# Performance work log

Measured on AMD Instinct MI355X. Metric: run time of the kernel, lower is better.

Reference implementation:

```python
import jax, jax.numpy as jnp
import numpy as np

T = 2048        # tokens
HID = 4096      # hidden_size
H = 32          # num attention heads
KV = 8          # num key/value heads (GQA)
D = HID // H    # head_dim = 128
THETA = 10000.0


def setup_inputs() -> dict:
    key = jax.random.key(0)
    k1, k2, k3 = jax.random.split(key, 3)
    hidden_states = jax.random.normal(k1, (T, HID), jnp.float32)
    positions = jnp.arange(T, dtype=jnp.int32)
    Wqkv = jax.random.normal(k2, ((H + 2 * KV) * D, HID), jnp.float32) * 0.02
    Wo = jax.random.normal(k3, (HID, H * D), jnp.float32) * 0.02
    return {"hidden_states": hidden_states, "positions": positions,
            "Wqkv": Wqkv, "Wo": Wo}


def _rope(positions, x):
    """Neox-style rotary embedding. x: [T, h, D], positions: [T]."""
    half = D // 2
    inv_freq = 1.0 / (THETA ** (jnp.arange(half, dtype=jnp.float32) / half))
    ang = positions.astype(jnp.float32)[:, None] * inv_freq      # [T, half]
    cos = jnp.cos(ang)[:, None, :]                                # [T, 1, half]
    sin = jnp.sin(ang)[:, None, :]
    x1, x2 = x[..., :half], x[..., half:]
    return jnp.concatenate([x1 * cos - x2 * sin, x2 * cos + x1 * sin], axis=-1)


def reference(hidden_states, positions, Wqkv, Wo):
    # fused QKV projection (no bias)
    qkv = hidden_states @ Wqkv.T                                  # [T, (H+2KV)*D]
    q, k, v = jnp.split(qkv, [H * D, H * D + KV * D], axis=1)
    q = q.reshape(T, H, D)
    k = k.reshape(T, KV, D)
    v = v.reshape(T, KV, D)
    # RoPE on q and k
    q = _rope(positions, q)
    k = _rope(positions, k)
    # GQA: expand kv heads to match q heads
    g = H // KV
    k = jnp.repeat(k, g, axis=1)                                  # [T, H, D]
    v = jnp.repeat(v, g, axis=1)
    # causal attention (flash-attention math)
    scores = jnp.einsum('thd,shd->hts', q, k) * (D ** -0.5)       # [H, T, T]
    causal = jnp.tril(jnp.ones((T, T), dtype=bool))
    scores = jnp.where(causal[None], scores, jnp.float32(-1e30))
    probs = jax.nn.softmax(scores, axis=-1)
    attn = jnp.einsum('hts,shd->thd', probs, v).reshape(T, H * D)
    # output projection
    return attn @ Wo.T
```

## Files before the change

kernel.cpp:

```cpp
#include <hip/hip_runtime.h>
#include <stdint.h>

#define T_SEQ 2048
#define HIDDEN 4096
#define NHEAD 32
#define NKV 8
#define HDIM 128
#define QKVN 6144

typedef __bf16 bf16x8 __attribute__((ext_vector_type(8)));
typedef float f32x4 __attribute__((ext_vector_type(4)));
typedef unsigned short u16;
typedef u16 u16x8 __attribute__((ext_vector_type(8)));
typedef u16 u16x4 __attribute__((ext_vector_type(4)));

__device__ __forceinline__ u16 f2bf(float f) {
  uint32_t u = __builtin_bit_cast(uint32_t, f);
  u = (u + 0x7fffu + ((u >> 16) & 1u)) >> 16;
  return (u16)u;
}
__device__ __forceinline__ float bf2f(u16 h) {
  uint32_t u = ((uint32_t)h) << 16;
  return __builtin_bit_cast(float, u);
}

__device__ __forceinline__ void gload16(const void* g, void* l) {
  __builtin_amdgcn_global_load_lds(
      (__attribute__((address_space(1))) void*)(uintptr_t)g,
      (__attribute__((address_space(3))) void*)(uintptr_t)l, 16, 0, 0);
}

__global__ void cvt_f32_bf16(const float* __restrict__ in, u16* __restrict__ out, int n) {
  int i = (blockIdx.x * blockDim.x + threadIdx.x) * 4;
  int stride = gridDim.x * blockDim.x * 4;
  for (; i < n; i += stride) {
    float4 v = *(const float4*)(in + i);
    u16x4 o;
    o.x = f2bf(v.x); o.y = f2bf(v.y); o.z = f2bf(v.z); o.w = f2bf(v.w);
    *(u16x4*)(out + i) = o;
  }
}

__global__ void rope_kernel(u16* __restrict__ qkv, const int* __restrict__ pos) {
  int idx = blockIdx.x * blockDim.x + threadIdx.x;
  if (idx >= T_SEQ * 40 * 64) return;
  int i = idx & 63;
  int head = (idx >> 6) % 40;
  int t = idx / (40 * 64);
  int base = head < NHEAD ? head * HDIM : NHEAD * HDIM + (head - NHEAD) * HDIM;
  float p = (float)pos[t];
  float inv_freq = exp2f(-(float)i * (13.287712379549449f / 64.0f));
  float ang = p * inv_freq;
  float s, c;
  sincosf(ang, &s, &c);
  u16* p1 = qkv + (size_t)t * QKVN + base + i;
  u16* p2 = p1 + 64;
  float x1 = bf2f(*p1), x2 = bf2f(*p2);
  *p1 = f2bf(x1 * c - x2 * s);
  *p2 = f2bf(x2 * c + x1 * s);
}

__device__ __forceinline__ void storeC(float* p, float v) { *p = v; }
__device__ __forceinline__ void storeC(u16* p, float v) { *p = f2bf(v); }

template <typename OutT>
__global__ void __launch_bounds__(256, 3)
gemm_k32(const u16* __restrict__ A, const u16* __restrict__ B,
         OutT* __restrict__ C, int M, int N, int K,
         int nbx, int rw, int rh) {
  __shared__ u16 As_[3][128 * 32];
  __shared__ u16 Bs_[3][128 * 32];

  const int tid = threadIdx.x;
  const int lane = tid & 63;
  const int w = tid >> 6;
  const int wr = w >> 1, wc = w & 1;
  const int l15 = lane & 15, lg = lane >> 4;

  const int c8 = blockIdx.x & 7;
  const int i8 = blockIdx.x >> 3;
  const int rpr = nbx / rw;
  const int by = (c8 / rpr) * rh + (i8 % rh);
  const int bx = (c8 % rpr) * rw + (i8 / rh);
  const int bm = by * 128, bn = bx * 128;

  const u16* asrc[2];
  const u16* bsrc[2];
#pragma unroll
  for (int g = 0; g < 2; ++g) {
    int u = g * 256 + w * 64 + lane;
    int r = u >> 2;
    int s = (u & 3) ^ (r & 3) ^ ((r >> 2) & 3);
    asrc[g] = A + (size_t)(bm + r) * K + s * 8;
    bsrc[g] = B + (size_t)(bn + r) * K + s * 8;
  }

  const int sl = (lg ^ (l15 & 3) ^ ((l15 >> 2) & 3)) * 8;
  const int a_rd = (wr * 64 + l15) * 32 + sl;
  const int b_rd = (wc * 64 + l15) * 32 + sl;

  f32x4 acc[4][4] = {};

#define BARRIER() asm volatile("s_barrier" ::: "memory")
#define WAITBAR(n_) asm volatile("s_waitcnt vmcnt(" #n_ ")\n\ts_barrier" ::: "memory")
#define STAGE(t_, p_)                                                          \
  {                                                                            \
    gload16(asrc[0] + (size_t)(t_) * 32, &As_[p_][w * 512]);                   \
    gload16(asrc[1] + (size_t)(t_) * 32, &As_[p_][2048 + w * 512]);            \
    gload16(bsrc[0] + (size_t)(t_) * 32, &Bs_[p_][w * 512]);                   \
    gload16(bsrc[1] + (size_t)(t_) * 32, &Bs_[p_][2048 + w * 512]);            \
  }

  STAGE(0, 0);
  STAGE(1, 1);
  WAITBAR(4);

  const int NT = K >> 5;
  int cur = 0;
  for (int t = 0; t < NT; ++t) {
    const int st = (cur == 0) ? 2 : cur - 1;
    if (t + 2 < NT) STAGE(t + 2, st);

    const u16* Ab = &As_[cur][a_rd];
    const u16* Bb = &Bs_[cur][b_rd];
    bf16x8 a0 = *(const bf16x8*)(Ab);
    bf16x8 a1 = *(const bf16x8*)(Ab + 512);
    bf16x8 a2 = *(const bf16x8*)(Ab + 1024);
    bf16x8 a3 = *(const bf16x8*)(Ab + 1536);
    __builtin_amdgcn_s_setprio(1);
#pragma unroll
    for (int ni = 0; ni < 4; ++ni) {
      bf16x8 b = *(const bf16x8*)(Bb + ni * 512);
      acc[0][ni] = __builtin_amdgcn_mfma_f32_16x16x32_bf16(a0, b, acc[0][ni], 0, 0, 0);
      acc[1][ni] = __builtin_amdgcn_mfma_f32_16x16x32_bf16(a1, b, acc[1][ni], 0, 0, 0);
      acc[2][ni] = __builtin_amdgcn_mfma_f32_16x16x32_bf16(a2, b, acc[2][ni], 0, 0, 0);
      acc[3][ni] = __builtin_amdgcn_mfma_f32_16x16x32_bf16(a3, b, acc[3][ni], 0, 0, 0);
    }
    __builtin_amdgcn_s_setprio(0);

    if (t + 2 < NT) {
      WAITBAR(4);
    } else if (t + 1 < NT) {
      WAITBAR(0);
    }
    cur = (cur == 2) ? 0 : cur + 1;
  }

#pragma unroll
  for (int mi = 0; mi < 4; ++mi)
#pragma unroll
    for (int ni = 0; ni < 4; ++ni)
#pragma unroll
      for (int r = 0; r < 4; ++r) {
        int row = bm + wr * 64 + mi * 16 + lg * 4 + r;
        int col = bn + wc * 64 + ni * 16 + l15;
        storeC(&C[(size_t)row * N + col], acc[mi][ni][r]);
      }
#undef STAGE
#undef WAITBAR
#undef BARRIER
}

__global__ void __launch_bounds__(256)
attn_kernel(const u16* __restrict__ qkv, u16* __restrict__ out) {
  __shared__ u16 Ksh[2][64 * 128];
  __shared__ u16 Vsh[2][128 * 64];
  __shared__ u16 Psh[4][16 * 64];

  const int tid = threadIdx.x;
  const int lane = tid & 63;
  const int w = tid >> 6;
  const int l15 = lane & 15, lg = lane >> 4;

  const int bid = blockIdx.x;
  const int kvh = bid & 7;
  const int hg = (bid >> 3) & 3;
  const int qi = 31 - (bid >> 5);
  const int h = kvh * 4 + hg;
  const int q0 = qi * 64;
  const int nt = qi + 1;

  const u16* Kg = qkv + NHEAD * HDIM + kvh * HDIM;
  const u16* Vg = qkv + (NHEAD + NKV) * HDIM + kvh * HDIM;

  bf16x8 qa[4];
  {
    const u16* qrow = qkv + (size_t)(q0 + w * 16 + l15) * QKVN + h * HDIM + lg * 8;
#pragma unroll
    for (int ks = 0; ks < 4; ++ks) qa[ks] = *(const bf16x8*)(qrow + ks * 32);
  }

  f32x4 acc_o[8] = {};
  float m[4], lsum[4];
#pragma unroll
  for (int r = 0; r < 4; ++r) { m[r] = -1e30f; lsum[r] = 0.f; }

  const float scale = 0.088388347648318447f;

#define STAGE_K(kv0, p)                                                        \
  {                                                                            \
    _Pragma("unroll") for (int rnd = 0; rnd < 4; ++rnd) {                      \
      int cc = rnd * 256 + tid;                                                \
      int krow = cc >> 4, kslot = cc & 15;                                     \
      gload16(Kg + (size_t)((kv0) + krow) * QKVN + (kslot ^ (krow & 7)) * 8,   \
              &Ksh[p][(rnd * 256 + w * 64) * 8]);                              \
    }                                                                          \
  }
#define LOAD_V(kv0, vr)                                                        \
  {                                                                            \
    _Pragma("unroll") for (int rnd = 0; rnd < 4; ++rnd) {                      \
      int cc = rnd * 256 + tid;                                                \
      int vrow = cc >> 4, d0 = (cc & 15) * 8;                                  \
      vr[rnd] = *(const u16x8*)(Vg + (size_t)((kv0) + vrow) * QKVN + d0);      \
    }                                                                          \
  }
#define WRITE_V(vr, p)                                                         \
  {                                                                            \
    _Pragma("unroll") for (int rnd = 0; rnd < 4; ++rnd) {                      \
      int cc = rnd * 256 + tid;                                                \
      int vrow = cc >> 4, d0 = (cc & 15) * 8;                                  \
      _Pragma("unroll") for (int j = 0; j < 8; ++j) {                          \
        int d = d0 + j;                                                        \
        Vsh[p][d * 64 + (((vrow >> 3) ^ (d & 7) ^ ((d >> 3) & 7)) * 8) +       \
               (vrow & 7)] = vr[rnd][j];                                       \
      }                                                                        \
    }                                                                          \
  }

  u16x8 vreg[4];
  STAGE_K(0, 0);
  LOAD_V(0, vreg);
  WRITE_V(vreg, 0);
  __syncthreads();

  for (int t = 0; t < nt; ++t) {
    const int p = t & 1;
    const int kv0 = t * 64;
    const bool more = (t + 1 < nt);
    u16x8 vnext[4];
    if (more) {
      STAGE_K(kv0 + 64, p ^ 1);
      LOAD_V(kv0 + 64, vnext);
    }

    f32x4 s[4] = {};
#pragma unroll
    for (int ks = 0; ks < 4; ++ks) {
#pragma unroll
      for (int n = 0; n < 4; ++n) {
        int row16 = n * 16 + l15;
        bf16x8 kf = *(const bf16x8*)&Ksh[p][row16 * 128 +
                                            (((ks * 4 + lg) ^ (row16 & 7)) * 8)];
        s[n] = __builtin_amdgcn_mfma_f32_16x16x32_bf16(qa[ks], kf, s[n], 0, 0, 0);
      }
    }

    const bool diag = (t == nt - 1);
    float alpha[4];
#pragma unroll
    for (int r = 0; r < 4; ++r) {
      int tq = q0 + w * 16 + lg * 4 + r;
      float mx = -1e30f;
#pragma unroll
      for (int n = 0; n < 4; ++n) {
        float v = s[n][r] * scale;
        if (diag && (kv0 + n * 16 + l15) > tq) v = -1e30f;
        s[n][r] = v;
        mx = fmaxf(mx, v);
      }
#pragma unroll
      for (int msk = 1; msk < 16; msk <<= 1) mx = fmaxf(mx, __shfl_xor(mx, msk, 64));
      float mn = fmaxf(m[r], mx);
      alpha[r] = __expf(m[r] - mn);
      m[r] = mn;
      float ps = 0.f;
#pragma unroll
      for (int n = 0; n < 4; ++n) {
        float pv = __expf(s[n][r] - mn);
        s[n][r] = pv;
        ps += pv;
      }
#pragma unroll
      for (int msk = 1; msk < 16; msk <<= 1) ps += __shfl_xor(ps, msk, 64);
      lsum[r] = lsum[r] * alpha[r] + ps;
      int prow = lg * 4 + r;
#pragma unroll
      for (int n = 0; n < 4; ++n)
        Psh[w][prow * 64 + (((n * 2 + (l15 >> 3)) ^ (prow & 7)) * 8) + (l15 & 7)] =
            f2bf(s[n][r]);
    }
#pragma unroll
    for (int f = 0; f < 8; ++f)
#pragma unroll
      for (int r = 0; r < 4; ++r) acc_o[f][r] *= alpha[r];

#pragma unroll
    for (int ks = 0; ks < 2; ++ks) {
      bf16x8 pa = *(const bf16x8*)&Psh[w][l15 * 64 + (((ks * 4 + lg) ^ (l15 & 7)) * 8)];
#pragma unroll
      for (int nd = 0; nd < 8; ++nd) {
        int d = nd * 16 + l15;
        bf16x8 bv = *(const bf16x8*)&Vsh[p][d * 64 +
                        (((ks * 4 + lg) ^ (d & 7) ^ ((d >> 3) & 7)) * 8)];
        acc_o[nd] = __builtin_amdgcn_mfma_f32_16x16x32_bf16(pa, bv, acc_o[nd], 0, 0, 0);
      }
    }

    if (more) WRITE_V(vnext, p ^ 1);
    __syncthreads();
  }

#pragma unroll
  for (int nd = 0; nd < 8; ++nd)
#pragma unroll
    for (int r = 0; r < 4; ++r) {
      int row = q0 + w * 16 + lg * 4 + r;
      int col = h * HDIM + nd * 16 + l15;
      out[(size_t)row * (NHEAD * HDIM) + col] = f2bf(acc_o[nd][r] / lsum[r]);
    }
#undef STAGE_K
#undef LOAD_V
#undef WRITE_V
}

extern "C" void kernel_launch(void* const* d_in, const int* in_sizes, int n_in,
                              void* d_out, int out_size, void* d_ws, size_t ws_size,
                              hipStream_t stream) {
  const float* hs   = (const float*)d_in[0];
  const int*   pos  = (const int*)d_in[1];
  const float* wqkv = (const float*)d_in[2];
  const float* wo   = (const float*)d_in[3];
  float* out = (float*)d_out;
  uint8_t* ws = (uint8_t*)d_ws;

  if (ws_size < 142606336u) return;
  u16* hs_bf   = (u16*)(ws + 0);
  u16* wqkv_bf = (u16*)(ws + 16777216u);
  u16* wo_bf   = (u16*)(ws + 67108864u);
  u16* qkv_bf  = (u16*)(ws + 100663296u);
  u16* attn_bf = (u16*)(ws + 125829120u);

  cvt_f32_bf16<<<2048, 256, 0, stream>>>(hs, hs_bf, T_SEQ * HIDDEN);
  cvt_f32_bf16<<<2048, 256, 0, stream>>>(wqkv, wqkv_bf, QKVN * HIDDEN);
  cvt_f32_bf16<<<2048, 256, 0, stream>>>(wo, wo_bf, HIDDEN * HIDDEN);

  gemm_k32<u16><<<768, 256, 0, stream>>>(hs_bf, wqkv_bf, qkv_bf,
                                         T_SEQ, QKVN, HIDDEN, 48, 12, 8);

  rope_kernel<<<(T_SEQ * 40 * 64) / 256, 256, 0, stream>>>(qkv_bf, pos);

  attn_kernel<<<1024, 256, 0, stream>>>(qkv_bf, attn_bf);

  gemm_k32<float><<<512, 256, 0, stream>>>(attn_bf, wo_bf, out,
                                           T_SEQ, HIDDEN, HIDDEN, 32, 8, 8);
}
```

Before: 373.9 us.

## Switch GEMMs to 256x256 tiles, fuse Wo conversion, split-K output projection

Replaces the 128x128 K32 GEMM with a 512-thread 256x256 tile kernel using K64 double-buffered LDS and staged interleaved loads between MFMA quads. The QKV GEMM grid also carries extra blocks that convert Wo to bf16 concurrently, removing a separate launch. The output projection uses split-K over two slices, writing a partial buffer that a reduce kernel adds into the output. This raises reuse per tile and fills the GPU with 256-block grids, at the cost of extra partial-sum traffic, a reduction pass, and higher LDS/register pressure.

```diff
diff --git a/kernel.cpp b/kernel.cpp
--- a/kernel.cpp
+++ b/kernel.cpp
@@ -62,103 +62,175 @@
 
 __device__ __forceinline__ void storeC(float* p, float v) { *p = v; }
 __device__ __forceinline__ void storeC(u16* p, float v) { *p = f2bf(v); }
-
-template <typename OutT>
-__global__ void __launch_bounds__(256, 3)
-gemm_k32(const u16* __restrict__ A, const u16* __restrict__ B,
-         OutT* __restrict__ C, int M, int N, int K,
-         int nbx, int rw, int rh) {
-  __shared__ u16 As_[3][128 * 32];
-  __shared__ u16 Bs_[3][128 * 32];
+__device__ __forceinline__ f32x4 mfma16(bf16x8 a, bf16x8 b, f32x4 c) {
+  return __builtin_amdgcn_mfma_f32_16x16x32_bf16(a, b, c, 0, 0, 0);
+}
+
+template <typename OutT, bool FUSED>
+__global__ void __launch_bounds__(512, 2)
+gemm256(const u16* __restrict__ A, const u16* __restrict__ B,
+        OutT* __restrict__ C0, OutT* __restrict__ C1,
+        int N, int K, int NT, int sliceBlocks, int nGemm,
+        int nbx, int rw, int rh,
+        const float* __restrict__ cvt_in, u16* __restrict__ cvt_out, int cvt_n4) {
+  if (FUSED && (int)blockIdx.x >= nGemm) {
+    int i = (blockIdx.x - nGemm) * blockDim.x + threadIdx.x;
+    int stride = (gridDim.x - nGemm) * blockDim.x;
+    for (; i < cvt_n4; i += stride) {
+      float4 v = ((const float4*)cvt_in)[i];
+      u16x4 o;
+      o.x = f2bf(v.x); o.y = f2bf(v.y); o.z = f2bf(v.z); o.w = f2bf(v.w);
+      ((u16x4*)cvt_out)[i] = o;
+    }
+    return;
+  }
+
+  __shared__ u16 As_[2][256 * 64];
+  __shared__ u16 Bs_[2][256 * 64];
 
   const int tid = threadIdx.x;
   const int lane = tid & 63;
   const int w = tid >> 6;
-  const int wr = w >> 1, wc = w & 1;
+  const int wr = w >> 2, wc = w & 3;
   const int l15 = lane & 15, lg = lane >> 4;
 
-  const int c8 = blockIdx.x & 7;
-  const int i8 = blockIdx.x >> 3;
+  const int bid = blockIdx.x;
+  const int slice = bid / sliceBlocks;
+  const int wi = bid % sliceBlocks;
+  const int k0 = slice * (NT << 6);
+  OutT* __restrict__ C = slice ? C1 : C0;
+
+  const int c8 = wi & 7, i8 = wi >> 3;
   const int rpr = nbx / rw;
   const int by = (c8 / rpr) * rh + (i8 % rh);
   const int bx = (c8 % rpr) * rw + (i8 / rh);
-  const int bm = by * 128, bn = bx * 128;
-
-  const u16* asrc[2];
-  const u16* bsrc[2];
-#pragma unroll
-  for (int g = 0; g < 2; ++g) {
-    int u = g * 256 + w * 64 + lane;
-    int r = u >> 2;
-    int s = (u & 3) ^ (r & 3) ^ ((r >> 2) & 3);
-    asrc[g] = A + (size_t)(bm + r) * K + s * 8;
-    bsrc[g] = B + (size_t)(bn + r) * K + s * 8;
-  }
-
-  const int sl = (lg ^ (l15 & 3) ^ ((l15 >> 2) & 3)) * 8;
-  const int a_rd = (wr * 64 + l15) * 32 + sl;
-  const int b_rd = (wc * 64 + l15) * 32 + sl;
-
-  f32x4 acc[4][4] = {};
+  const int bm = by * 256, bn = bx * 256;
+
+  const int u_lo = w * 64 + lane, u_hi = u_lo + 512;
+  const int r0 = u_lo >> 3, s0 = (u_lo & 7) ^ (r0 & 7);
+  const int r1 = u_hi >> 3, s1 = (u_hi & 7) ^ (r1 & 7);
+  const u16* a0s0 = A + (size_t)(bm + r0) * K + k0 + s0 * 8;
+  const u16* a0s1 = A + (size_t)(bm + r1) * K + k0 + s1 * 8;
+  const u16* a1s0 = A + (size_t)(bm + 128 + r0) * K + k0 + s0 * 8;
+  const u16* a1s1 = A + (size_t)(bm + 128 + r1) * K + k0 + s1 * 8;
+  const u16* b0s0 = B + (size_t)(bn + r0) * K + k0 + s0 * 8;
+  const u16* b0s1 = B + (size_t)(bn + r1) * K + k0 + s1 * 8;
+  const u16* b1s0 = B + (size_t)(bn + 128 + r0) * K + k0 + s0 * 8;
+  const u16* b1s1 = B + (size_t)(bn + 128 + r1) * K + k0 + s1 * 8;
+
+  const int ax = l15 & 7;
+  const int sl0 = (lg ^ ax) * 8;
+  const int sl1 = ((4 + lg) ^ ax) * 8;
+  const int a_row = (wr * 128 + l15) * 64;
+  const int b_row = (wc * 64 + l15) * 64;
+
+  f32x4 acc[8][4] = {};
+  bf16x8 bfr[4][2];
 
 #define BARRIER() asm volatile("s_barrier" ::: "memory")
 #define WAITBAR(n_) asm volatile("s_waitcnt vmcnt(" #n_ ")\n\ts_barrier" ::: "memory")
-#define STAGE(t_, p_)                                                          \
+#define STAGE_HALF(p0_, p1_, dst_, t_)                                         \
   {                                                                            \
-    gload16(asrc[0] + (size_t)(t_) * 32, &As_[p_][w * 512]);                   \
-    gload16(asrc[1] + (size_t)(t_) * 32, &As_[p_][2048 + w * 512]);            \
-    gload16(bsrc[0] + (size_t)(t_) * 32, &Bs_[p_][w * 512]);                   \
-    gload16(bsrc[1] + (size_t)(t_) * 32, &Bs_[p_][2048 + w * 512]);            \
-  }
-
-  STAGE(0, 0);
-  STAGE(1, 1);
+    gload16((p0_) + (size_t)(t_) * 64, (dst_) + (size_t)w * 512);              \
+    gload16((p1_) + (size_t)(t_) * 64, (dst_) + 4096 + (size_t)w * 512);       \
+  }
+
+  STAGE_HALF(a0s0, a0s1, &As_[0][0], 0);
+  STAGE_HALF(a1s0, a1s1, &As_[0][8192], 0);
+  STAGE_HALF(b0s0, b0s1, &Bs_[0][0], 0);
+  STAGE_HALF(b1s0, b1s1, &Bs_[0][8192], 0);
+  STAGE_HALF(b0s0, b0s1, &Bs_[1][0], 1);
+  STAGE_HALF(b1s0, b1s1, &Bs_[1][8192], 1);
   WAITBAR(4);
 
-  const int NT = K >> 5;
-  int cur = 0;
-  for (int t = 0; t < NT; ++t) {
-    const int st = (cur == 0) ? 2 : cur - 1;
-    if (t + 2 < NT) STAGE(t + 2, st);
-
-    const u16* Ab = &As_[cur][a_rd];
-    const u16* Bb = &Bs_[cur][b_rd];
-    bf16x8 a0 = *(const bf16x8*)(Ab);
-    bf16x8 a1 = *(const bf16x8*)(Ab + 512);
-    bf16x8 a2 = *(const bf16x8*)(Ab + 1024);
-    bf16x8 a3 = *(const bf16x8*)(Ab + 1536);
-    __builtin_amdgcn_s_setprio(1);
-#pragma unroll
-    for (int ni = 0; ni < 4; ++ni) {
-      bf16x8 b = *(const bf16x8*)(Bb + ni * 512);
-      acc[0][ni] = __builtin_amdgcn_mfma_f32_16x16x32_bf16(a0, b, acc[0][ni], 0, 0, 0);
-      acc[1][ni] = __builtin_amdgcn_mfma_f32_16x16x32_bf16(a1, b, acc[1][ni], 0, 0, 0);
-      acc[2][ni] = __builtin_amdgcn_mfma_f32_16x16x32_bf16(a2, b, acc[2][ni], 0, 0, 0);
-      acc[3][ni] = __builtin_amdgcn_mfma_f32_16x16x32_bf16(a3, b, acc[3][ni], 0, 0, 0);
-    }
+  for (int v = 0; v < NT; ++v) {
+    const int cur = v & 1, alt = cur ^ 1;
+    const u16* Ac = &As_[cur][0];
+    const u16* Bc = &Bs_[cur][0];
+    const bool s1ok = (v + 1) < NT, s2ok = (v + 2) < NT;
+
+#define MFMA_QUAD(p_, A0_, A1_, A2_, A3_)                                      \
+    __builtin_amdgcn_s_setprio(1);                                             \
+    _Pragma("unroll") for (int ni = 0; ni < 4; ++ni) {                         \
+      acc[2 * (p_)][ni] = mfma16(A0_, bfr[ni][0], acc[2 * (p_)][ni]);          \
+      acc[2 * (p_)][ni] = mfma16(A1_, bfr[ni][1], acc[2 * (p_)][ni]);          \
+      acc[2 * (p_) + 1][ni] = mfma16(A2_, bfr[ni][0], acc[2 * (p_) + 1][ni]);  \
+      acc[2 * (p_) + 1][ni] = mfma16(A3_, bfr[ni][1], acc[2 * (p_) + 1][ni]);  \
+    }                                                                          \
     __builtin_amdgcn_s_setprio(0);
 
-    if (t + 2 < NT) {
-      WAITBAR(4);
-    } else if (t + 1 < NT) {
-      WAITBAR(0);
-    }
-    cur = (cur == 2) ? 0 : cur + 1;
-  }
-
-#pragma unroll
-  for (int mi = 0; mi < 4; ++mi)
+    {
+#pragma unroll
+      for (int ni = 0; ni < 4; ++ni) {
+        bfr[ni][0] = *(const bf16x8*)&Bc[b_row + ni * 1024 + sl0];
+        bfr[ni][1] = *(const bf16x8*)&Bc[b_row + ni * 1024 + sl1];
+      }
+      bf16x8 f0 = *(const bf16x8*)&Ac[a_row + 0 * 1024 + sl0];
+      bf16x8 f1 = *(const bf16x8*)&Ac[a_row + 0 * 1024 + sl1];
+      bf16x8 f2 = *(const bf16x8*)&Ac[a_row + 1 * 1024 + sl0];
+      bf16x8 f3 = *(const bf16x8*)&Ac[a_row + 1 * 1024 + sl1];
+      if (s1ok) STAGE_HALF(a0s0, a0s1, &As_[alt][0], v + 1);
+      BARRIER();
+      MFMA_QUAD(0, f0, f1, f2, f3);
+      BARRIER();
+    }
+    {
+      bf16x8 f0 = *(const bf16x8*)&Ac[a_row + 2 * 1024 + sl0];
+      bf16x8 f1 = *(const bf16x8*)&Ac[a_row + 2 * 1024 + sl1];
+      bf16x8 f2 = *(const bf16x8*)&Ac[a_row + 3 * 1024 + sl0];
+      bf16x8 f3 = *(const bf16x8*)&Ac[a_row + 3 * 1024 + sl1];
+      if (s1ok) STAGE_HALF(a1s0, a1s1, &As_[alt][8192], v + 1);
+      if (s2ok) STAGE_HALF(b0s0, b0s1, &Bs_[cur][0], v + 2);
+      BARRIER();
+      MFMA_QUAD(1, f0, f1, f2, f3);
+      BARRIER();
+    }
+    {
+      bf16x8 f0 = *(const bf16x8*)&Ac[a_row + 4 * 1024 + sl0];
+      bf16x8 f1 = *(const bf16x8*)&Ac[a_row + 4 * 1024 + sl1];
+      bf16x8 f2 = *(const bf16x8*)&Ac[a_row + 5 * 1024 + sl0];
+      bf16x8 f3 = *(const bf16x8*)&Ac[a_row + 5 * 1024 + sl1];
+      if (s2ok) STAGE_HALF(b1s0, b1s1, &Bs_[cur][8192], v + 2);
+      BARRIER();
+      MFMA_QUAD(2, f0, f1, f2, f3);
+      BARRIER();
+    }
+    {
+      bf16x8 f0 = *(const bf16x8*)&Ac[a_row + 6 * 1024 + sl0];
+      bf16x8 f1 = *(const bf16x8*)&Ac[a_row + 6 * 1024 + sl1];
+      bf16x8 f2 = *(const bf16x8*)&Ac[a_row + 7 * 1024 + sl0];
+      bf16x8 f3 = *(const bf16x8*)&Ac[a_row + 7 * 1024 + sl1];
+      BARRIER();
+      MFMA_QUAD(3, f0, f1, f2, f3);
+      if (s2ok) { WAITBAR(4); } else { WAITBAR(0); }
+    }
+#undef MFMA_QUAD
+  }
+
+#pragma unroll
+  for (int mi = 0; mi < 8; ++mi)
 #pragma unroll
     for (int ni = 0; ni < 4; ++ni)
 #pragma unroll
       for (int r = 0; r < 4; ++r) {
-        int row = bm + wr * 64 + mi * 16 + lg * 4 + r;
+        int row = bm + wr * 128 + mi * 16 + lg * 4 + r;
         int col = bn + wc * 64 + ni * 16 + l15;
         storeC(&C[(size_t)row * N + col], acc[mi][ni][r]);
       }
-#undef STAGE
+#undef STAGE_HALF
 #undef WAITBAR
 #undef BARRIER
+}
+
+__global__ void reduce_add(float* __restrict__ out, const float* __restrict__ part, int n4) {
+  int i = blockIdx.x * blockDim.x + threadIdx.x;
+  int stride = gridDim.x * blockDim.x;
+  for (; i < n4; i += stride) {
+    float4 a = ((const float4*)out)[i];
+    float4 b = ((const float4*)part)[i];
+    a.x += b.x; a.y += b.y; a.z += b.z; a.w += b.w;
+    ((float4*)out)[i] = a;
+  }
 }
 
 __global__ void __launch_bounds__(256)
@@ -339,18 +411,22 @@
   u16* wo_bf   = (u16*)(ws + 67108864u);
   u16* qkv_bf  = (u16*)(ws + 100663296u);
   u16* attn_bf = (u16*)(ws + 125829120u);
+  float* part  = (float*)(ws + 16777216u);
 
   cvt_f32_bf16<<<2048, 256, 0, stream>>>(hs, hs_bf, T_SEQ * HIDDEN);
   cvt_f32_bf16<<<2048, 256, 0, stream>>>(wqkv, wqkv_bf, QKVN * HIDDEN);
-  cvt_f32_bf16<<<2048, 256, 0, stream>>>(wo, wo_bf, HIDDEN * HIDDEN);
-
-  gemm_k32<u16><<<768, 256, 0, stream>>>(hs_bf, wqkv_bf, qkv_bf,
-                                         T_SEQ, QKVN, HIDDEN, 48, 12, 8);
+
+  gemm256<u16, true><<<256, 512, 0, stream>>>(
+      hs_bf, wqkv_bf, qkv_bf, qkv_bf, QKVN, HIDDEN, 64,
+      192, 192, 24, 3, 8, wo, wo_bf, (HIDDEN * HIDDEN) / 4);
 
   rope_kernel<<<(T_SEQ * 40 * 64) / 256, 256, 0, stream>>>(qkv_bf, pos);
 
   attn_kernel<<<1024, 256, 0, stream>>>(qkv_bf, attn_bf);
 
-  gemm_k32<float><<<512, 256, 0, stream>>>(attn_bf, wo_bf, out,
-                                           T_SEQ, HIDDEN, HIDDEN, 32, 8, 8);
-}
+  gemm256<float, false><<<256, 512, 0, stream>>>(
+      attn_bf, wo_bf, out, part, HIDDEN, HIDDEN, 32,
+      128, 256, 16, 2, 8, nullptr, nullptr, 0);
+
+  reduce_add<<<2048, 256, 0, stream>>>(out, part, (T_SEQ * HIDDEN) / 4);
+}
```

After: 353.9 us. -5.3%, faster.
